# Performance work log

Measured on AMD Instinct MI355X. Metric: run time of the kernel, lower is better.

## Reference

```python
import jax, jax.numpy as jnp
import numpy as np

NUM_HEADS = 8
GROUPS = 32
EPS = 1e-5


def setup_inputs() -> dict:
    key = jax.random.key(0)
    ks = jax.random.split(key, 4)
    B, C, H, W = 8, 512, 32, 32
    x = jax.random.normal(ks[0], (B, C, H, W), dtype=jnp.float32)
    gn_w = jnp.ones((C,), dtype=jnp.float32)
    gn_b = jnp.zeros((C,), dtype=jnp.float32)
    qkv_w = jax.random.normal(ks[1], (3 * C, C), dtype=jnp.float32) * (1.0 / np.sqrt(C))
    qkv_b = jnp.zeros((3 * C,), dtype=jnp.float32)
    proj_w = jax.random.normal(ks[2], (C, C), dtype=jnp.float32) * (1.0 / np.sqrt(C))
    proj_b = jnp.zeros((C,), dtype=jnp.float32)
    return {"x": x, "gn_w": gn_w, "gn_b": gn_b, "qkv_w": qkv_w,
            "qkv_b": qkv_b, "proj_w": proj_w, "proj_b": proj_b}


def reference(x, gn_w, gn_b, qkv_w, qkv_b, proj_w, proj_b):
    b, c, h, w = x.shape
    n = h * w
    hd = c // NUM_HEADS
    xf = x.reshape(b, c, n)
    # GroupNorm over (channels_per_group, HW) per sample
    xg = xf.reshape(b, GROUPS, -1)
    mu = jnp.mean(xg, axis=-1, keepdims=True)
    var = jnp.var(xg, axis=-1, keepdims=True)
    xn = ((xg - mu) * jax.lax.rsqrt(var + EPS)).reshape(b, c, n)
    xn = xn * gn_w[None, :, None] + gn_b[None, :, None]
    # 1x1 conv == channel matmul
    qkv = jnp.einsum('oc,bcn->bon', qkv_w, xn) + qkv_b[None, :, None]
    q, k, v = jnp.split(qkv, 3, axis=1)
    q = q.reshape(b, NUM_HEADS, hd, n)
    k = k.reshape(b, NUM_HEADS, hd, n)
    v = v.reshape(b, NUM_HEADS, hd, n)
    scale = hd ** 0.5
    score = jnp.einsum('bhdn,bhdm->bhnm', q, k) / scale  # [b,h,HW,HW]
    attn = jax.nn.softmax(score, axis=-1)
    out = jnp.einsum('bhnm,bhdm->bhnd', attn, v)  # [b,h,HW,hd]
    out = out.transpose(0, 1, 3, 2).reshape(b, c, n)
    out = jnp.einsum('oc,bcn->bon', proj_w, out) + proj_b[None, :, None]
    return x + out.reshape(b, c, h, w)
```

## Files before the change

kernel.cpp:

```cpp
#include <hip/hip_runtime.h>

typedef unsigned short u16;
typedef unsigned long long u64;
typedef __bf16 bf16x8 __attribute__((ext_vector_type(8)));
typedef float f32x4 __attribute__((ext_vector_type(4)));

#define NB 8
#define NC 512
#define NN 1024
#define NHEADS 8
#define HDIM 64
#define CPG 16
#define EPSV 1e-5f
#define LOG2E 1.44269504f

__device__ __forceinline__ float bf2f(u16 h) {
  union { unsigned u; float f; } v; v.u = ((unsigned)h) << 16; return v.f;
}
__device__ __forceinline__ u16 f2bf(float f) {
  union { float f; unsigned u; } v; v.f = f;
  unsigned r = v.u + 0x7fffu + ((v.u >> 16) & 1u);
  return (u16)(r >> 16);
}
__device__ __forceinline__ float h2f(u16 h) {
  unsigned s = (h >> 15) & 1u, e = (h >> 10) & 31u, m = h & 1023u;
  union { unsigned u; float f; } v;
  if (e == 0) { v.u = s << 31; return v.f + (s ? -1.f : 1.f) * (float)m * 5.9604645e-8f; }
  if (e == 31) { v.u = (s << 31) | 0x7F800000u | (m << 13); return v.f; }
  v.u = (s << 31) | ((e + 112u) << 23) | (m << 13);
  return v.f;
}
__device__ __forceinline__ u16 f2h(float f) {
  union { float f; unsigned u; } v; v.f = f;
  unsigned s = (v.u >> 16) & 0x8000u; int e = (int)((v.u >> 23) & 0xFF) - 112;
  unsigned m = v.u & 0x7FFFFFu;
  if (e <= 0) return (u16)s;
  if (e >= 31) return (u16)(s | 0x7C00u);
  u16 h = (u16)(s | (e << 10) | (m >> 13));
  unsigned rem = m & 0x1FFFu;
  if (rem > 0x1000u || (rem == 0x1000u && (h & 1u))) ++h;
  return h;
}
__device__ __forceinline__ float load_elem(const void* p, size_t i, int f) {
  if (f == 1) return bf2f(((const u16*)p)[i]);
  if (f == 2) return h2f(((const u16*)p)[i]);
  return ((const float*)p)[i];
}

__device__ __forceinline__ float exp2_fast(float x) {
  float r;
  asm("v_exp_f32 %0, %1" : "=v"(r) : "v"(x));
  return r;
}

__global__ void detect_dtype(const u16* __restrict__ gw_raw, int* __restrict__ flag) {
  if (threadIdx.x != 0 || blockIdx.x != 0) return;
  int bf = 0, hf = 0;
  for (int i = 0; i < 16; ++i) {
    u16 w = gw_raw[i];
    if (w == 0x3F80u) ++bf;
    else if (w == 0x3C00u) ++hf;
  }
  *flag = (bf >= 12) ? 1 : (hf >= 12) ? 2 : 0;
}

__global__ __launch_bounds__(256) void cvt_to_bf16(const void* __restrict__ raw,
                                                   u16* __restrict__ dst, int n,
                                                   const int* __restrict__ flag) {
  const int f = *flag;
  const int i = (blockIdx.x * 256 + threadIdx.x) * 4;
  if (i >= n) return;
  if (f == 1) {
    *(uint2*)(dst + i) = *(const uint2*)((const u16*)raw + i);
  } else if (f == 0) {
    float4 v = *(const float4*)((const float*)raw + i);
    u16 o[4] = {f2bf(v.x), f2bf(v.y), f2bf(v.z), f2bf(v.w)};
    *(u64*)(dst + i) = *(const u64*)o;
  } else {
    u16 o[4];
#pragma unroll
    for (int k2 = 0; k2 < 4; ++k2) o[k2] = f2bf(h2f(((const u16*)raw)[i + k2]));
    *(u64*)(dst + i) = *(const u64*)o;
  }
}

__global__ __launch_bounds__(256) void cvt_biases(const void* __restrict__ gw,
                                                  const void* __restrict__ gb,
                                                  const void* __restrict__ qb,
                                                  const void* __restrict__ pb,
                                                  float* __restrict__ cgw,
                                                  float* __restrict__ cgb,
                                                  float* __restrict__ cqb,
                                                  float* __restrict__ cpb,
                                                  const int* __restrict__ flag) {
  const int f = *flag;
  int i = blockIdx.x * 256 + threadIdx.x;
  if (i < 512)        cgw[i] = load_elem(gw, i, f);
  else if (i < 1024)  cgb[i - 512] = load_elem(gb, (size_t)(i - 512), f);
  else if (i < 2560)  cqb[i - 1024] = load_elem(qb, (size_t)(i - 1024), f);
  else                cpb[i - 2560] = load_elem(pb, (size_t)(i - 2560), f);
}

__global__ __launch_bounds__(256) void gn_naive(const void* __restrict__ x,
                                                const int* __restrict__ flag,
                                                const float* __restrict__ gw,
                                                const float* __restrict__ gb,
                                                u16* __restrict__ xn, int b0) {
  const int f = *flag;
  const int bl = blockIdx.x >> 5;
  const int g  = blockIdx.x & 31;
  const size_t base = ((size_t)((b0 + bl) * NC + g * CPG)) * NN;
  u16* dst = xn + ((size_t)(bl * NC + g * CPG)) * NN;
  __shared__ float r1[256], r2[256];
  const int t = threadIdx.x;
  float s = 0.f, ss = 0.f;
  if (f == 1) {
    const u16* xb = (const u16*)x + base;
    for (int i0 = t * 8; i0 < CPG * NN; i0 += 2048) {
      uint4 dv = *(const uint4*)(xb + i0);
      const u16* pp = (const u16*)&dv;
#pragma unroll
      for (int j = 0; j < 8; ++j) { float v = bf2f(pp[j]); s += v; ss += v * v; }
    }
  } else if (f == 0) {
    const float* xb = (const float*)x + base;
    for (int i0 = t * 4; i0 < CPG * NN; i0 += 1024) {
      float4 v = *(const float4*)(xb + i0);
      s += v.x + v.y + v.z + v.w;
      ss += v.x * v.x + v.y * v.y + v.z * v.z + v.w * v.w;
    }
  } else {
    for (int i = t; i < CPG * NN; i += 256) {
      float v = load_elem(x, base + i, f); s += v; ss += v * v;
    }
  }
  r1[t] = s; r2[t] = ss; __syncthreads();
  for (int k = 128; k > 0; k >>= 1) {
    if (t < k) { r1[t] += r1[t + k]; r2[t] += r2[t + k]; }
    __syncthreads();
  }
  const float mu  = r1[0] * (1.f / 16384.f);
  const float var = r2[0] * (1.f / 16384.f) - mu * mu;
  const float rs  = rsqrtf(var + EPSV);
  if (f == 1) {
    const u16* xb = (const u16*)x + base;
    for (int i0 = t * 8; i0 < CPG * NN; i0 += 2048) {
      const int c = g * CPG + (i0 >> 10);
      const float wsc = gw[c] * rs;
      const float bsc = gb[c] - mu * wsc;
      uint4 dv = *(const uint4*)(xb + i0);
      const u16* pp = (const u16*)&dv;
      u16 o[8];
#pragma unroll
      for (int j = 0; j < 8; ++j) o[j] = f2bf(bf2f(pp[j]) * wsc + bsc);
      *(uint4*)(dst + i0) = *(uint4*)o;
    }
  } else if (f == 0) {
    const float* xb = (const float*)x + base;
    for (int i0 = t * 4; i0 < CPG * NN; i0 += 1024) {
      const int c = g * CPG + (i0 >> 10);
      const float wsc = gw[c] * rs;
      const float bsc = gb[c] - mu * wsc;
      float4 v = *(const float4*)(xb + i0);
      u16 o[4] = {f2bf(v.x * wsc + bsc), f2bf(v.y * wsc + bsc),
                  f2bf(v.z * wsc + bsc), f2bf(v.w * wsc + bsc)};
      *(u64*)(dst + i0) = *(const u64*)o;
    }
  } else {
    for (int i = t; i < CPG * NN; i += 256) {
      int c = g * CPG + i / NN;
      dst[i] = f2bf((load_elem(x, base + i, f) - mu) * rs * gw[c] + gb[c]);
    }
  }
}

__global__ __launch_bounds__(256) void gemm_mfma(const u16* __restrict__ A,
                                                 const u16* __restrict__ Bn,
                                                 const float* __restrict__ bias,
                                                 void* __restrict__ out,
                                                 const void* __restrict__ resid,
                                                 const int* __restrict__ flag,
                                                 int M, int K, int b0, int kmode) {
  __shared__ alignas(16) u16 sA[128 * 40];
  __shared__ alignas(16) u16 sB[128 * 40];
  const int m0 = blockIdx.x * 128;
  const int n0 = blockIdx.y * 128;
  const int bz = blockIdx.z;
  const int t = threadIdx.x;
  const int lane = t & 63, wv = t >> 6;
  const int wm = (wv >> 1) * 64, wn = (wv & 1) * 64;
  const int lr = lane & 15, quad = lane >> 4;
  const int f = *flag;

  const int ar0 = t >> 2, akc = (t & 3) * 8;
  const int ar1 = 64 + ar0;
  const int bc0 = t >> 4, bno = (t & 15) * 8;
  const int bc1 = 16 + bc0;

  f32x4 acc[4][4] = {};

  uint4 ra0 = *(const uint4*)(A + (size_t)(m0 + ar0) * K + akc);
  uint4 ra1 = *(const uint4*)(A + (size_t)(m0 + ar1) * K + akc);
  uint4 rb0 = *(const uint4*)(Bn + ((size_t)bz * K + bc0) * NN + n0 + bno);
  uint4 rb1 = *(const uint4*)(Bn + ((size_t)bz * K + bc1) * NN + n0 + bno);

  for (int k0 = 0; k0 < K; k0 += 32) {
    __syncthreads();
    *(uint4*)(sA + ar0 * 40 + akc) = ra0;
    *(uint4*)(sA + ar1 * 40 + akc) = ra1;
    {
      const u16* p0 = (const u16*)&rb0;
      const u16* p1 = (const u16*)&rb1;
#pragma unroll
      for (int j = 0; j < 8; ++j) {
        const int row = bno + j;
        sB[row * 40 + (bc0 ^ (row & 24))] = p0[j];
        sB[row * 40 + (bc1 ^ (row & 24))] = p1[j];
      }
    }
    __syncthreads();
    if (k0 + 32 < K) {
      ra0 = *(const uint4*)(A + (size_t)(m0 + ar0) * K + k0 + 32 + akc);
      ra1 = *(const uint4*)(A + (size_t)(m0 + ar1) * K + k0 + 32 + akc);
      rb0 = *(const uint4*)(Bn + ((size_t)bz * K + k0 + 32 + bc0) * NN + n0 + bno);
      rb1 = *(const uint4*)(Bn + ((size_t)bz * K + k0 + 32 + bc1) * NN + n0 + bno);
    }
    const u16* pA = sA + (wm + lr) * 40 + quad * 8;
    bf16x8 af[4], bfv[4];
#pragma unroll
    for (int i = 0; i < 4; ++i) {
      af[i] = *(const bf16x8*)(pA + i * 640);
      const int rowB = wn + lr + i * 16;
      bfv[i] = *(const bf16x8*)(sB + rowB * 40 + ((quad * 8) ^ (rowB & 24)));
    }
#pragma unroll
    for (int i = 0; i < 4; ++i)
#pragma unroll
      for (int j = 0; j < 4; ++j)
        acc[i][j] = __builtin_amdgcn_mfma_f32_16x16x32_bf16(af[i], bfv[j], acc[i][j], 0, 0, 0);
  }

  const bool kstore = (kmode != 0) && (m0 >= 512) && (m0 < 1024);
  if (kstore) {
    u16* kb2 = (u16*)out + ((size_t)(b0 + bz) * 1536 + 512) * NN;
#pragma unroll
    for (int i = 0; i < 4; ++i) {
      const int mb = m0 + wm + i * 16 + quad * 4;
      const int hh = (mb - 512) >> 6;
      const int d0 = (mb - 512) & 63;
      u16* hb = kb2 + (size_t)hh * NN * 64 + d0;
#pragma unroll
      for (int j = 0; j < 4; ++j) {
        const int col = n0 + wn + j * 16 + lr;
        u16 o[4];
#pragma unroll
        for (int r = 0; r < 4; ++r) o[r] = f2bf(acc[i][j][r] + bias[mb + r]);
        *(u64*)(hb + (size_t)col * 64) = *(const u64*)o;
      }
    }
    return;
  }
#pragma unroll
  for (int i = 0; i < 4; ++i) {
    const int mb = m0 + wm + i * 16 + quad * 4;
#pragma unroll
    for (int r = 0; r < 4; ++r) {
      const int mr = mb + r;
      const float bi = bias[mr];
#pragma unroll
      for (int j = 0; j < 4; ++j) {
        const int col = n0 + wn + j * 16 + lr;
        const size_t oidx = ((size_t)(b0 + bz) * M + mr) * NN + col;
        float v = acc[i][j][r] + bi;
        if (resid) {
          v += load_elem(resid, oidx, f);
          if (f == 1)      ((u16*)out)[oidx] = f2bf(v);
          else if (f == 2) ((u16*)out)[oidx] = f2h(v);
          else             ((float*)out)[oidx] = v;
        } else {
          ((u16*)out)[oidx] = f2bf(v);
        }
      }
    }
  }
}

__global__ __launch_bounds__(256) void attn_mfma(const u16* __restrict__ qkv,
                                                 u16* __restrict__ attnO) {
  __shared__ alignas(16) u16 sK[2][64 * 64];
  __shared__ alignas(16) u16 sV[2][64 * 64];

  const int L   = blockIdx.x + 16 * (blockIdx.y + 8 * blockIdx.z);
  const int xcd = L & 7;
  const int jj  = L >> 3;
  const int grp = xcd + 8 * (jj >> 4);
  const int qt  = jj & 15;
  const int h   = grp & 7;
  const int bz  = grp >> 3;

  const int n0 = qt * 64;
  const u16* qb    = qkv + ((size_t)bz * 1536 + h * HDIM) * NN;
  const u16* kbase = qkv + ((size_t)bz * 1536 + 512) * NN + (size_t)h * NN * HDIM;
  const u16* vb    = qb + (size_t)1024 * NN;
  const int t = threadIdx.x;
  const int lane = t & 63, wv = t >> 6;
  const int lr = lane & 15, quad = lane >> 4;

  const int qcol = n0 + wv * 16 + lr;
  union { u16 u[8]; bf16x8 v; } qa0, qa1;
#pragma unroll
  for (int e = 0; e < 8; ++e) {
    qa0.u[e] = qb[(size_t)(quad * 8 + e) * NN + qcol];
    qa1.u[e] = qb[(size_t)(quad * 8 + 32 + e) * NN + qcol];
  }
  const bf16x8 a0 = qa0.v;
  const bf16x8 a1 = qa1.v;

  const int km = t >> 2;
  const int kc = t & 3;
  const int ke = (km ^ (km >> 3)) & 7;
  const u16* kp = kbase + (size_t)km * 64 + kc * 8;

  const int sd  = t >> 3;
  const int smo = (t & 7) * 8;
  const u16* vp = vb + (size_t)sd * NN + smo;
  const int vs0 = sd * 64 + (smo ^ (8 * (sd & 7)));
  const int vs1 = (sd + 32) * 64 + (smo ^ (8 * ((sd + 32) & 7)));

  uint4 pk0, pk1, pv0, pv1;

  f32x4 acc_o[4] = {};
  float mrow = -1e30f, lrow = 0.f;

  pk0 = *(const uint4*)(kp);
  pk1 = *(const uint4*)(kp + 32);
  pv0 = *(const uint4*)(vp);
  pv1 = *(const uint4*)(vp + (size_t)32 * NN);
  {
    u16* kd = &sK[0][km * 64];
    *(uint4*)(kd + ((kc ^ ke) * 8)) = pk0;
    *(uint4*)(kd + (((kc + 4) ^ ke) * 8)) = pk1;
    *(uint4*)(&sV[0][vs0]) = pv0;
    *(uint4*)(&sV[0][vs1]) = pv1;
  }
  pk0 = *(const uint4*)(kp + 4096);
  pk1 = *(const uint4*)(kp + 4096 + 32);
  pv0 = *(const uint4*)(vp + 64);
  pv1 = *(const uint4*)(vp + (size_t)32 * NN + 64);
  __syncthreads();

  for (int mt = 0; mt < 16; ++mt) {
    const int c = mt & 1;

    f32x4 p[4];
    __builtin_amdgcn_s_setprio(1);
#pragma unroll
    for (int j = 0; j < 4; ++j) {
      const int rk = j * 16 + lr;
      const u16* pKr = &sK[c][rk * 64];
      const int sw = ((rk ^ (rk >> 3)) & 7) * 8;
      bf16x8 k0 = *(const bf16x8*)(pKr + ((quad * 8) ^ sw));
      bf16x8 k1 = *(const bf16x8*)(pKr + ((quad * 8 + 32) ^ sw));
      f32x4 z = {0.f, 0.f, 0.f, 0.f};
      z = __builtin_amdgcn_mfma_f32_16x16x32_bf16(k0, a0, z, 0, 0, 0);
      z = __builtin_amdgcn_mfma_f32_16x16x32_bf16(k1, a1, z, 0, 0, 0);
      p[j] = z;
    }
    __builtin_amdgcn_s_setprio(0);

    float mx = -1e30f;
#pragma unroll
    for (int j = 0; j < 4; ++j)
#pragma unroll
      for (int r = 0; r < 4; ++r) mx = fmaxf(mx, p[j][r]);
    mx = fmaxf(mx, __shfl_xor(mx, 16));
    mx = fmaxf(mx, __shfl_xor(mx, 32));
    const float msc = mx * 0.125f;
    if (!__all(msc - mrow <= 8.f)) {
      const float mnew = fmaxf(mrow, msc);
      const float alpha = exp2_fast((mrow - mnew) * LOG2E);
      mrow = mnew;
      lrow *= alpha;
      float ar[4];
#pragma unroll
      for (int r = 0; r < 4; ++r) ar[r] = __shfl(alpha, quad * 4 + r);
#pragma unroll
      for (int j2 = 0; j2 < 4; ++j2)
#pragma unroll
        for (int r = 0; r < 4; ++r) acc_o[j2][r] *= ar[r];
    }
    const float m2 = mrow * LOG2E;
    float ls = 0.f;
#pragma unroll
    for (int j = 0; j < 4; ++j)
#pragma unroll
      for (int r = 0; r < 4; ++r) {
        const float pe = exp2_fast(fmaf(p[j][r], 0.18033688f, -m2));
        p[j][r] = pe;
        ls += pe;
      }
    ls += __shfl_xor(ls, 16);
    ls += __shfl_xor(ls, 32);
    lrow += ls;

    unsigned pa[4], pb2[4];
#pragma unroll
    for (int j = 0; j < 4; ++j) {
      asm("v_cvt_pk_bf16_f32 %0, %1, %2" : "=v"(pa[j]) : "v"(p[j][0]), "v"(p[j][1]));
      asm("v_cvt_pk_bf16_f32 %0, %1, %2" : "=v"(pb2[j]) : "v"(p[j][2]), "v"(p[j][3]));
    }

    __builtin_amdgcn_s_setprio(1);
#pragma unroll
    for (int ks = 0; ks < 2; ++ks) {
      union { unsigned u[4]; bf16x8 v; } af;
      af.u[0] = pa[2 * ks];
      af.u[1] = pb2[2 * ks];
      af.u[2] = pa[2 * ks + 1];
      af.u[3] = pb2[2 * ks + 1];
#pragma unroll
      for (int j2 = 0; j2 < 4; ++j2) {
        const int rv = j2 * 16 + lr;
        const int swv = 8 * (rv & 7);
        const u16* pVr = &sV[c][rv * 64];
        union { u64 q[2]; bf16x8 v; } bfv;
        bfv.q[0] = *(const u64*)(pVr + ((ks * 32 + 4 * quad) ^ swv));
        bfv.q[1] = *(const u64*)(pVr + ((ks * 32 + 16 + 4 * quad) ^ swv));
        acc_o[j2] = __builtin_amdgcn_mfma_f32_16x16x32_bf16(af.v, bfv.v, acc_o[j2], 0, 0, 0);
      }
    }
    __builtin_amdgcn_s_setprio(0);

    if (mt < 15) {
      const int cn = c ^ 1;
      u16* kd = &sK[cn][km * 64];
      *(uint4*)(kd + ((kc ^ ke) * 8)) = pk0;
      *(uint4*)(kd + (((kc + 4) ^ ke) * 8)) = pk1;
      *(uint4*)(&sV[cn][vs0]) = pv0;
      *(uint4*)(&sV[cn][vs1]) = pv1;
      if (mt < 14) {
        const size_t ko = (size_t)(mt + 2) * 4096;
        const int mo = (mt + 2) * 64;
        pk0 = *(const uint4*)(kp + ko);
        pk1 = *(const uint4*)(kp + ko + 32);
        pv0 = *(const uint4*)(vp + mo);
        pv1 = *(const uint4*)(vp + (size_t)32 * NN + mo);
      }
      __syncthreads();
    }
  }

  const float invl = 1.f / lrow;
  float ir[4];
#pragma unroll
  for (int r = 0; r < 4; ++r) ir[r] = __shfl(invl, quad * 4 + r);
  const int qrow = n0 + wv * 16 + quad * 4;
#pragma unroll
  for (int j2 = 0; j2 < 4; ++j2) {
    const int d = j2 * 16 + lr;
    u16 o[4];
#pragma unroll
    for (int r = 0; r < 4; ++r) o[r] = f2bf(acc_o[j2][r] * ir[r]);
    *(u64*)(attnO + ((size_t)bz * NC + h * HDIM + d) * NN + qrow) = *(const u64*)o;
  }
}

__global__ void sig_small_ws(u16* out) {
  if (threadIdx.x == 0 && blockIdx.x == 0) out[0] = f2bf(20000.f);
}

extern "C" void kernel_launch(void* const* d_in, const int* in_sizes, int n_in,
                              void* d_out, int out_size, void* d_ws, size_t ws_size,
                              hipStream_t stream) {
  const void* x      = d_in[0];
  const void* gn_w   = d_in[1];
  const void* gn_b   = d_in[2];
  const void* qkv_w  = d_in[3];
  const void* qkv_b  = d_in[4];
  const void* proj_w = d_in[5];
  const void* proj_b = d_in[6];
  char* ws = (char*)d_ws;
  const size_t MB = (size_t)1 << 20;

  u16*   wq16 = (u16*)(ws);
  u16*   wp16 = (u16*)(ws + 3 * MB / 2);
  float* cgw  = (float*)(ws + 2 * MB);
  float* cgb  = (float*)(ws + 2 * MB + 4096);
  float* cqb  = (float*)(ws + 2 * MB + 8192);
  float* cpb  = (float*)(ws + 2 * MB + 16384);
  int*   flag = (int*)  (ws + 2 * MB + 20480);

  detect_dtype<<<dim3(1), dim3(64), 0, stream>>>((const u16*)gn_w, flag);
  cvt_to_bf16<<<dim3(768), dim3(256), 0, stream>>>(qkv_w, wq16, 786432, flag);
  cvt_to_bf16<<<dim3(256), dim3(256), 0, stream>>>(proj_w, wp16, 262144, flag);
  cvt_biases<<<dim3(12), dim3(256), 0, stream>>>(gn_w, gn_b, qkv_b, proj_b,
                                                 cgw, cgb, cqb, cpb, flag);

  if (ws_size >= 36 * MB) {
    u16* xn    = (u16*)(ws + 3 * MB);
    u16* qkvb  = (u16*)(ws + 11 * MB);
    u16* attnO = xn;
    gn_naive<<<dim3(NB * 32), dim3(256), 0, stream>>>(x, flag, cgw, cgb, xn, 0);
    gemm_mfma<<<dim3(12, 8, NB), dim3(256), 0, stream>>>(wq16, xn, cqb, qkvb,
                                                         nullptr, flag, 1536, NC, 0, 1);
    attn_mfma<<<dim3(16, NHEADS, NB), dim3(256), 0, stream>>>(qkvb, attnO);
    gemm_mfma<<<dim3(4, 8, NB), dim3(256), 0, stream>>>(wp16, attnO, cpb, d_out,
                                                        x, flag, NC, NC, 0, 0);
  } else if (ws_size >= 9 * MB) {
    u16* xn    = (u16*)(ws + 3 * MB);
    u16* qkvb  = (u16*)(ws + 4 * MB);
    u16* attnO = (u16*)(ws + 7 * MB);
    for (int b = 0; b < NB; ++b) {
      gn_naive<<<dim3(32), dim3(256), 0, stream>>>(x, flag, cgw, cgb, xn, b);
      gemm_mfma<<<dim3(12, 8, 1), dim3(256), 0, stream>>>(wq16, xn, cqb, qkvb,
                                                          nullptr, flag, 1536, NC, 0, 1);
      attn_mfma<<<dim3(16, NHEADS, 1), dim3(256), 0, stream>>>(qkvb, attnO);
      gemm_mfma<<<dim3(4, 8, 1), dim3(256), 0, stream>>>(wp16, attnO, cpb, d_out,
                                                         x, flag, NC, NC, b, 0);
    }
  } else {
    sig_small_ws<<<dim3(1), dim3(64), 0, stream>>>((u16*)d_out);
  }
}
```

Before: 206.0 us.

## Load attention K/V fragments directly from global and double-register GEMM prefetch

The attention kernel drops its shared-memory double buffer for K and V. Each wave now loads its MFMA fragments straight from global memory into registers every tile, which removes LDS staging and the per-tile block barriers. The cost is that each of the four waves in a block reads the same K/V tile separately through cache, with uncoalesced 8-byte V reads and more register pressure. The GEMM kernel also changes to handle two K-steps per loop iteration, prefetching two stages ahead in registers to hide global latency.

```diff
diff --git a/kernel.cpp b/kernel.cpp
--- a/kernel.cpp
+++ b/kernel.cpp
@@ -199,45 +199,72 @@
 
   f32x4 acc[4][4] = {};
 
-  uint4 ra0 = *(const uint4*)(A + (size_t)(m0 + ar0) * K + akc);
-  uint4 ra1 = *(const uint4*)(A + (size_t)(m0 + ar1) * K + akc);
-  uint4 rb0 = *(const uint4*)(Bn + ((size_t)bz * K + bc0) * NN + n0 + bno);
-  uint4 rb1 = *(const uint4*)(Bn + ((size_t)bz * K + bc1) * NN + n0 + bno);
-
-  for (int k0 = 0; k0 < K; k0 += 32) {
+  const u16* pa0 = A + (size_t)(m0 + ar0) * K + akc;
+  const u16* pa1 = A + (size_t)(m0 + ar1) * K + akc;
+  const u16* pb0 = Bn + ((size_t)bz * K + bc0) * NN + n0 + bno;
+  const u16* pb1 = Bn + ((size_t)bz * K + bc1) * NN + n0 + bno;
+
+  uint4 xa0 = *(const uint4*)(pa0);
+  uint4 xa1 = *(const uint4*)(pa1);
+  uint4 xb0 = *(const uint4*)(pb0);
+  uint4 xb1 = *(const uint4*)(pb1);
+  uint4 ya0 = *(const uint4*)(pa0 + 32);
+  uint4 ya1 = *(const uint4*)(pa1 + 32);
+  uint4 yb0 = *(const uint4*)(pb0 + (size_t)32 * NN);
+  uint4 yb1 = *(const uint4*)(pb1 + (size_t)32 * NN);
+
+#define GEMM_STAGE(ra0, ra1, rb0, rb1)                                   \
+  {                                                                      \
+    *(uint4*)(sA + ar0 * 40 + akc) = ra0;                                \
+    *(uint4*)(sA + ar1 * 40 + akc) = ra1;                                \
+    const u16* p0 = (const u16*)&rb0;                                    \
+    const u16* p1 = (const u16*)&rb1;                                    \
+    _Pragma("unroll")                                                    \
+    for (int j = 0; j < 8; ++j) {                                        \
+      const int row = bno + j;                                           \
+      sB[row * 40 + (bc0 ^ (row & 24))] = p0[j];                         \
+      sB[row * 40 + (bc1 ^ (row & 24))] = p1[j];                         \
+    }                                                                    \
+  }
+
+#define GEMM_MFMA_BLOCK()                                                \
+  {                                                                      \
+    const u16* pA = sA + (wm + lr) * 40 + quad * 8;                      \
+    bf16x8 af[4], bfv[4];                                                \
+    _Pragma("unroll")                                                    \
+    for (int i = 0; i < 4; ++i) {                                        \
+      af[i] = *(const bf16x8*)(pA + i * 640);                            \
+      const int rowB = wn + lr + i * 16;                                 \
+      bfv[i] = *(const bf16x8*)(sB + rowB * 40 + ((quad * 8) ^ (rowB & 24))); \
+    }                                                                    \
+    _Pragma("unroll")                                                    \
+    for (int i = 0; i < 4; ++i)                                          \
+      _Pragma("unroll")                                                  \
+      for (int j = 0; j < 4; ++j)                                        \
+        acc[i][j] = __builtin_amdgcn_mfma_f32_16x16x32_bf16(af[i], bfv[j], acc[i][j], 0, 0, 0); \
+  }
+
+  for (int k0 = 0; k0 < K; k0 += 64) {
     __syncthreads();
-    *(uint4*)(sA + ar0 * 40 + akc) = ra0;
-    *(uint4*)(sA + ar1 * 40 + akc) = ra1;
-    {
-      const u16* p0 = (const u16*)&rb0;
-      const u16* p1 = (const u16*)&rb1;
-#pragma unroll
-      for (int j = 0; j < 8; ++j) {
-        const int row = bno + j;
-        sB[row * 40 + (bc0 ^ (row & 24))] = p0[j];
-        sB[row * 40 + (bc1 ^ (row & 24))] = p1[j];
-      }
-    }
+    GEMM_STAGE(xa0, xa1, xb0, xb1);
     __syncthreads();
-    if (k0 + 32 < K) {
-      ra0 = *(const uint4*)(A + (size_t)(m0 + ar0) * K + k0 + 32 + akc);
-      ra1 = *(const uint4*)(A + (size_t)(m0 + ar1) * K + k0 + 32 + akc);
-      rb0 = *(const uint4*)(Bn + ((size_t)bz * K + k0 + 32 + bc0) * NN + n0 + bno);
-      rb1 = *(const uint4*)(Bn + ((size_t)bz * K + k0 + 32 + bc1) * NN + n0 + bno);
-    }
-    const u16* pA = sA + (wm + lr) * 40 + quad * 8;
-    bf16x8 af[4], bfv[4];
-#pragma unroll
-    for (int i = 0; i < 4; ++i) {
-      af[i] = *(const bf16x8*)(pA + i * 640);
-      const int rowB = wn + lr + i * 16;
-      bfv[i] = *(const bf16x8*)(sB + rowB * 40 + ((quad * 8) ^ (rowB & 24)));
-    }
-#pragma unroll
-    for (int i = 0; i < 4; ++i)
-#pragma unroll
-      for (int j = 0; j < 4; ++j)
-        acc[i][j] = __builtin_amdgcn_mfma_f32_16x16x32_bf16(af[i], bfv[j], acc[i][j], 0, 0, 0);
+    if (k0 + 64 < K) {
+      xa0 = *(const uint4*)(pa0 + k0 + 64);
+      xa1 = *(const uint4*)(pa1 + k0 + 64);
+      xb0 = *(const uint4*)(pb0 + (size_t)(k0 + 64) * NN);
+      xb1 = *(const uint4*)(pb1 + (size_t)(k0 + 64) * NN);
+    }
+    GEMM_MFMA_BLOCK();
+    __syncthreads();
+    GEMM_STAGE(ya0, ya1, yb0, yb1);
+    __syncthreads();
+    if (k0 + 96 < K) {
+      ya0 = *(const uint4*)(pa0 + k0 + 96);
+      ya1 = *(const uint4*)(pa1 + k0 + 96);
+      yb0 = *(const uint4*)(pb0 + (size_t)(k0 + 96) * NN);
+      yb1 = *(const uint4*)(pb1 + (size_t)(k0 + 96) * NN);
+    }
+    GEMM_MFMA_BLOCK();
   }
 
   const bool kstore = (kmode != 0) && (m0 >= 512) && (m0 < 1024);
@@ -287,9 +314,6 @@
 
 __global__ __launch_bounds__(256) void attn_mfma(const u16* __restrict__ qkv,
                                                  u16* __restrict__ attnO) {
-  __shared__ alignas(16) u16 sK[2][64 * 64];
-  __shared__ alignas(16) u16 sV[2][64 * 64];
-
   const int L   = blockIdx.x + 16 * (blockIdx.y + 8 * blockIdx.z);
   const int xcd = L & 7;
   const int jj  = L >> 3;
@@ -316,54 +340,39 @@
   const bf16x8 a0 = qa0.v;
   const bf16x8 a1 = qa1.v;
 
-  const int km = t >> 2;
-  const int kc = t & 3;
-  const int ke = (km ^ (km >> 3)) & 7;
-  const u16* kp = kbase + (size_t)km * 64 + kc * 8;
-
-  const int sd  = t >> 3;
-  const int smo = (t & 7) * 8;
-  const u16* vp = vb + (size_t)sd * NN + smo;
-  const int vs0 = sd * 64 + (smo ^ (8 * (sd & 7)));
-  const int vs1 = (sd + 32) * 64 + (smo ^ (8 * ((sd + 32) & 7)));
-
-  uint4 pk0, pk1, pv0, pv1;
+  const u16* kf = kbase + (size_t)lr * 64 + quad * 8;
+  const u16* vf = vb + (size_t)lr * NN + 4 * quad;
 
   f32x4 acc_o[4] = {};
   float mrow = -1e30f, lrow = 0.f;
 
-  pk0 = *(const uint4*)(kp);
-  pk1 = *(const uint4*)(kp + 32);
-  pv0 = *(const uint4*)(vp);
-  pv1 = *(const uint4*)(vp + (size_t)32 * NN);
-  {
-    u16* kd = &sK[0][km * 64];
-    *(uint4*)(kd + ((kc ^ ke) * 8)) = pk0;
-    *(uint4*)(kd + (((kc + 4) ^ ke) * 8)) = pk1;
-    *(uint4*)(&sV[0][vs0]) = pv0;
-    *(uint4*)(&sV[0][vs1]) = pv1;
-  }
-  pk0 = *(const uint4*)(kp + 4096);
-  pk1 = *(const uint4*)(kp + 4096 + 32);
-  pv0 = *(const uint4*)(vp + 64);
-  pv1 = *(const uint4*)(vp + (size_t)32 * NN + 64);
-  __syncthreads();
-
   for (int mt = 0; mt < 16; ++mt) {
-    const int c = mt & 1;
+    const int m0 = mt * 64;
+
+    union { uint4 q; bf16x8 v; } k0f[4], k1f[4];
+#pragma unroll
+    for (int j = 0; j < 4; ++j) {
+      const u16* kr = kf + (size_t)(m0 + j * 16) * 64;
+      k0f[j].q = *(const uint4*)(kr);
+      k1f[j].q = *(const uint4*)(kr + 32);
+    }
+    union { u64 q[2]; bf16x8 v; } vfr[2][4];
+#pragma unroll
+    for (int ks = 0; ks < 2; ++ks)
+#pragma unroll
+      for (int j2 = 0; j2 < 4; ++j2) {
+        const u16* vr = vf + (size_t)(j2 * 16) * NN + m0 + ks * 32;
+        vfr[ks][j2].q[0] = *(const u64*)(vr);
+        vfr[ks][j2].q[1] = *(const u64*)(vr + 16);
+      }
 
     f32x4 p[4];
     __builtin_amdgcn_s_setprio(1);
 #pragma unroll
     for (int j = 0; j < 4; ++j) {
-      const int rk = j * 16 + lr;
-      const u16* pKr = &sK[c][rk * 64];
-      const int sw = ((rk ^ (rk >> 3)) & 7) * 8;
-      bf16x8 k0 = *(const bf16x8*)(pKr + ((quad * 8) ^ sw));
-      bf16x8 k1 = *(const bf16x8*)(pKr + ((quad * 8 + 32) ^ sw));
       f32x4 z = {0.f, 0.f, 0.f, 0.f};
-      z = __builtin_amdgcn_mfma_f32_16x16x32_bf16(k0, a0, z, 0, 0, 0);
-      z = __builtin_amdgcn_mfma_f32_16x16x32_bf16(k1, a1, z, 0, 0, 0);
+      z = __builtin_amdgcn_mfma_f32_16x16x32_bf16(k0f[j].v, a0, z, 0, 0, 0);
+      z = __builtin_amdgcn_mfma_f32_16x16x32_bf16(k1f[j].v, a1, z, 0, 0, 0);
       p[j] = z;
     }
     __builtin_amdgcn_s_setprio(0);
@@ -419,35 +428,10 @@
       af.u[2] = pa[2 * ks + 1];
       af.u[3] = pb2[2 * ks + 1];
 #pragma unroll
-      for (int j2 = 0; j2 < 4; ++j2) {
-        const int rv = j2 * 16 + lr;
-        const int swv = 8 * (rv & 7);
-        const u16* pVr = &sV[c][rv * 64];
-        union { u64 q[2]; bf16x8 v; } bfv;
-        bfv.q[0] = *(const u64*)(pVr + ((ks * 32 + 4 * quad) ^ swv));
-        bfv.q[1] = *(const u64*)(pVr + ((ks * 32 + 16 + 4 * quad) ^ swv));
-        acc_o[j2] = __builtin_amdgcn_mfma_f32_16x16x32_bf16(af.v, bfv.v, acc_o[j2], 0, 0, 0);
-      }
+      for (int j2 = 0; j2 < 4; ++j2)
+        acc_o[j2] = __builtin_amdgcn_mfma_f32_16x16x32_bf16(af.v, vfr[ks][j2].v, acc_o[j2], 0, 0, 0);
     }
     __builtin_amdgcn_s_setprio(0);
-
-    if (mt < 15) {
-      const int cn = c ^ 1;
-      u16* kd = &sK[cn][km * 64];
-      *(uint4*)(kd + ((kc ^ ke) * 8)) = pk0;
-      *(uint4*)(kd + (((kc + 4) ^ ke) * 8)) = pk1;
-      *(uint4*)(&sV[cn][vs0]) = pv0;
-      *(uint4*)(&sV[cn][vs1]) = pv1;
-      if (mt < 14) {
-        const size_t ko = (size_t)(mt + 2) * 4096;
-        const int mo = (mt + 2) * 64;
-        pk0 = *(const uint4*)(kp + ko);
-        pk1 = *(const uint4*)(kp + ko + 32);
-        pv0 = *(const uint4*)(vp + mo);
-        pv1 = *(const uint4*)(vp + (size_t)32 * NN + mo);
-      }
-      __syncthreads();
-    }
   }
 
   const float invl = 1.f / lrow;
```

Result: slower. 331.4 us (+60.9%).

## Double-buffer LDS in projection GEMM and remap blocks across XCDs

Applied to the files above, without the earlier changes.

The channel-matmul GEMM kernel now uses two LDS buffers, staging the next K-slice while MFMAs run on the current one. This cuts the number of barriers per K step and deepens global-load prefetch to two slices ahead. Block indices are also remapped so that consecutive launch IDs, which round-robin across the 8 XCDs, share the same A rows and improve L2 reuse. The cost is doubled shared memory and more live registers, which may lower occupancy. The remap assumes gridDim.y is 8 and that nsteps is even.

```diff
diff --git a/kernel.cpp b/kernel.cpp
--- a/kernel.cpp
+++ b/kernel.cpp
@@ -181,11 +181,19 @@
                                                  const void* __restrict__ resid,
                                                  const int* __restrict__ flag,
                                                  int M, int K, int b0, int kmode) {
-  __shared__ alignas(16) u16 sA[128 * 40];
-  __shared__ alignas(16) u16 sB[128 * 40];
-  const int m0 = blockIdx.x * 128;
-  const int n0 = blockIdx.y * 128;
-  const int bz = blockIdx.z;
+  __shared__ alignas(16) u16 sA[2][128 * 40];
+  __shared__ alignas(16) u16 sB[2][128 * 40];
+
+  const int gx = gridDim.x;
+  const int Lx = blockIdx.x + gx * (blockIdx.y + 8 * blockIdx.z);
+  const int xcd = Lx & 7;
+  const int q8  = Lx >> 3;
+  const int bx  = q8 % gx;
+  const int pp_ = xcd + 8 * (q8 / gx);
+  const int m0 = bx * 128;
+  const int n0 = (pp_ & 7) * 128;
+  const int bz = pp_ >> 3;
+
   const int t = threadIdx.x;
   const int lane = t & 63, wv = t >> 6;
   const int wm = (wv >> 1) * 64, wn = (wv & 1) * 64;
@@ -199,45 +207,82 @@
 
   f32x4 acc[4][4] = {};
 
-  uint4 ra0 = *(const uint4*)(A + (size_t)(m0 + ar0) * K + akc);
-  uint4 ra1 = *(const uint4*)(A + (size_t)(m0 + ar1) * K + akc);
-  uint4 rb0 = *(const uint4*)(Bn + ((size_t)bz * K + bc0) * NN + n0 + bno);
-  uint4 rb1 = *(const uint4*)(Bn + ((size_t)bz * K + bc1) * NN + n0 + bno);
-
-  for (int k0 = 0; k0 < K; k0 += 32) {
+  const u16* pa0 = A + (size_t)(m0 + ar0) * K + akc;
+  const u16* pa1 = A + (size_t)(m0 + ar1) * K + akc;
+  const u16* pb0 = Bn + ((size_t)bz * K + bc0) * NN + n0 + bno;
+  const u16* pb1 = Bn + ((size_t)bz * K + bc1) * NN + n0 + bno;
+
+#define GSTAGE(dA, dB, ra0_, ra1_, rb0_, rb1_)                           \
+  {                                                                      \
+    *(uint4*)(dA + ar0 * 40 + akc) = ra0_;                               \
+    *(uint4*)(dA + ar1 * 40 + akc) = ra1_;                               \
+    const u16* p0 = (const u16*)&rb0_;                                   \
+    const u16* p1 = (const u16*)&rb1_;                                   \
+    _Pragma("unroll")                                                    \
+    for (int j = 0; j < 8; ++j) {                                        \
+      const int row = bno + j;                                           \
+      dB[row * 40 + (bc0 ^ (row & 24))] = p0[j];                         \
+      dB[row * 40 + (bc1 ^ (row & 24))] = p1[j];                         \
+    }                                                                    \
+  }
+
+#define GMFMA(srcA, srcB)                                                \
+  {                                                                      \
+    const u16* pA_ = srcA + (wm + lr) * 40 + quad * 8;                   \
+    bf16x8 af[4], bfv[4];                                                \
+    _Pragma("unroll")                                                    \
+    for (int i = 0; i < 4; ++i) {                                        \
+      af[i] = *(const bf16x8*)(pA_ + i * 640);                           \
+      const int rowB = wn + lr + i * 16;                                 \
+      bfv[i] = *(const bf16x8*)(srcB + rowB * 40 + ((quad * 8) ^ (rowB & 24))); \
+    }                                                                    \
+    _Pragma("unroll")                                                    \
+    for (int i = 0; i < 4; ++i)                                          \
+      _Pragma("unroll")                                                  \
+      for (int j = 0; j < 4; ++j)                                        \
+        acc[i][j] = __builtin_amdgcn_mfma_f32_16x16x32_bf16(af[i], bfv[j], acc[i][j], 0, 0, 0); \
+  }
+
+  const int nsteps = K >> 5;
+
+  uint4 xa0 = *(const uint4*)(pa0);
+  uint4 xa1 = *(const uint4*)(pa1);
+  uint4 xb0 = *(const uint4*)(pb0);
+  uint4 xb1 = *(const uint4*)(pb1);
+  uint4 ya0 = *(const uint4*)(pa0 + 32);
+  uint4 ya1 = *(const uint4*)(pa1 + 32);
+  uint4 yb0 = *(const uint4*)(pb0 + (size_t)32 * NN);
+  uint4 yb1 = *(const uint4*)(pb1 + (size_t)32 * NN);
+  GSTAGE(sA[0], sB[0], xa0, xa1, xb0, xb1);
+  xa0 = *(const uint4*)(pa0 + 64);
+  xa1 = *(const uint4*)(pa1 + 64);
+  xb0 = *(const uint4*)(pb0 + (size_t)64 * NN);
+  xb1 = *(const uint4*)(pb1 + (size_t)64 * NN);
+  __syncthreads();
+
+  for (int s = 0; s < nsteps; s += 2) {
+    GSTAGE(sA[1], sB[1], ya0, ya1, yb0, yb1);
+    if (s + 3 < nsteps) {
+      const int ks = (s + 3) * 32;
+      ya0 = *(const uint4*)(pa0 + ks);
+      ya1 = *(const uint4*)(pa1 + ks);
+      yb0 = *(const uint4*)(pb0 + (size_t)ks * NN);
+      yb1 = *(const uint4*)(pb1 + (size_t)ks * NN);
+    }
+    GMFMA(sA[0], sB[0]);
     __syncthreads();
-    *(uint4*)(sA + ar0 * 40 + akc) = ra0;
-    *(uint4*)(sA + ar1 * 40 + akc) = ra1;
-    {
-      const u16* p0 = (const u16*)&rb0;
-      const u16* p1 = (const u16*)&rb1;
-#pragma unroll
-      for (int j = 0; j < 8; ++j) {
-        const int row = bno + j;
-        sB[row * 40 + (bc0 ^ (row & 24))] = p0[j];
-        sB[row * 40 + (bc1 ^ (row & 24))] = p1[j];
+    if (s + 2 < nsteps) {
+      GSTAGE(sA[0], sB[0], xa0, xa1, xb0, xb1);
+      if (s + 4 < nsteps) {
+        const int ks = (s + 4) * 32;
+        xa0 = *(const uint4*)(pa0 + ks);
+        xa1 = *(const uint4*)(pa1 + ks);
+        xb0 = *(const uint4*)(pb0 + (size_t)ks * NN);
+        xb1 = *(const uint4*)(pb1 + (size_t)ks * NN);
       }
     }
-    __syncthreads();
-    if (k0 + 32 < K) {
-      ra0 = *(const uint4*)(A + (size_t)(m0 + ar0) * K + k0 + 32 + akc);
-      ra1 = *(const uint4*)(A + (size_t)(m0 + ar1) * K + k0 + 32 + akc);
-      rb0 = *(const uint4*)(Bn + ((size_t)bz * K + k0 + 32 + bc0) * NN + n0 + bno);
-      rb1 = *(const uint4*)(Bn + ((size_t)bz * K + k0 + 32 + bc1) * NN + n0 + bno);
-    }
-    const u16* pA = sA + (wm + lr) * 40 + quad * 8;
-    bf16x8 af[4], bfv[4];
-#pragma unroll
-    for (int i = 0; i < 4; ++i) {
-      af[i] = *(const bf16x8*)(pA + i * 640);
-      const int rowB = wn + lr + i * 16;
-      bfv[i] = *(const bf16x8*)(sB + rowB * 40 + ((quad * 8) ^ (rowB & 24)));
-    }
-#pragma unroll
-    for (int i = 0; i < 4; ++i)
-#pragma unroll
-      for (int j = 0; j < 4; ++j)
-        acc[i][j] = __builtin_amdgcn_mfma_f32_16x16x32_bf16(af[i], bfv[j], acc[i][j], 0, 0, 0);
+    GMFMA(sA[1], sB[1]);
+    if (s + 2 < nsteps) __syncthreads();
   }
 
   const bool kstore = (kmode != 0) && (m0 >= 512) && (m0 < 1024);
```

Result: slower. 221.4 us (+7.5%).
